# Kernel optimization log

Measured on AMD Instinct MI355X. Metric: run time of the kernel, lower is better.

The kernel has to match this reference:

```python
import jax, jax.numpy as jnp
import numpy as np

RES = 256      # cubic grid resolution
CH = 16        # feature channels
RR = 8         # reduced_res = ceil(log2(RES))
MASK = 128     # low-frequency mask size
N_PTS = 262144 # query points


def _bilinear(feat, gx, gy):
    """torch.F.grid_sample, bilinear, align_corners=True, zero padding.
    feat: (C,H,W); gx,gy: (N,) in [-1,1] (gx indexes W, gy indexes H).
    Returns (N,C)."""
    H, W = feat.shape[1], feat.shape[2]
    x = (gx + 1.0) * 0.5 * (W - 1)
    y = (gy + 1.0) * 0.5 * (H - 1)
    x0 = jnp.floor(x)
    y0 = jnp.floor(y)
    wx = x - x0
    wy = y - y0
    x0i = jnp.clip(x0.astype(jnp.int32), 0, W - 1)
    x1i = jnp.clip(x0i + 1, 0, W - 1)
    y0i = jnp.clip(y0.astype(jnp.int32), 0, H - 1)
    y1i = jnp.clip(y0i + 1, 0, H - 1)
    v00 = feat[:, y0i, x0i]
    v01 = feat[:, y0i, x1i]
    v10 = feat[:, y1i, x0i]
    v11 = feat[:, y1i, x1i]
    out = (v00 * (1 - wx) * (1 - wy) + v01 * wx * (1 - wy)
           + v10 * (1 - wx) * wy + v11 * wx * wy)  # (C,N)
    return out.T


def _plane(P, mask2d, gx, gy, icoord):
    """One phasor plane: mask -> ifft2 -> grid_sample -> Fourier integration.
    P: (CH*RR, RES, RES, 2); returns (N, CH)."""
    Pc = (P[..., 0] + 1j * P[..., 1]) * mask2d          # (C,H,W) complex
    Pc = jnp.fft.ifft2(Pc)                              # ifft over last 2 axes
    C = P.shape[0]
    # interleave (real, imag) per complex channel, like permute+reshape in torch
    feat = jnp.stack([Pc.real, Pc.imag], axis=1).reshape(2 * C, RES, RES)
    samp = _bilinear(feat, gx, gy).reshape(-1, 2 * CH, RR)  # (N, 2*CH, RR)
    Z = samp[:, :CH] + 1j * samp[:, CH:]                    # (N, CH, RR)
    s = (icoord + 1.0) * 0.5 * (2 ** RR - 1)                # scaled coord
    coef = 2.0 ** jnp.arange(RR) - 1.0                      # (RR,)
    basis = jnp.exp(2j * jnp.pi * s[:, None] * coef / (2 ** RR))  # (N, RR)
    return jnp.einsum('nr,ncr->nc', basis, Z).real


def _forward(Pu, Pv, Pw, inputs):
    mask2d = jnp.zeros((RES, RES), jnp.float32).at[:MASK, :MASK].set(1.0)
    out = (_plane(Pu, mask2d, inputs[:, 1], inputs[:, 2], inputs[:, 0])
           + _plane(Pv, mask2d, inputs[:, 0], inputs[:, 2], inputs[:, 1])
           + _plane(Pw, mask2d, inputs[:, 0], inputs[:, 1], inputs[:, 2]))
    return out  # (N, CH)


def setup_inputs() -> dict:
    key = jax.random.key(0)
    k1, k2, k3, k4 = jax.random.split(key, 4)
    Pu = 0.001 * jax.random.normal(k1, (CH * RR, RES, RES, 2), jnp.float32)
    Pv = 0.001 * jax.random.normal(k2, (CH * RR, RES, RES, 2), jnp.float32)
    Pw = 0.001 * jax.random.normal(k3, (CH * RR, RES, RES, 2), jnp.float32)
    inputs = jax.random.uniform(k4, (N_PTS, 3), jnp.float32, -1.0, 1.0)
    return {"Pu": Pu, "Pv": Pv, "Pw": Pw, "inputs": inputs}


def reference(Pu, Pv, Pw, inputs):
    return _forward(Pu, Pv, Pw, inputs)
```

## Files before the change

kernel.cpp:

```cpp
#include <hip/hip_runtime.h>
#include <hip/hip_bf16.h>
#include <cmath>


#define NPTS 262144

typedef float vf2 __attribute__((ext_vector_type(2)));

__device__ __forceinline__ int brev8(int x) { return (int)(__brev((unsigned)x) >> 24); }

__device__ __forceinline__ unsigned pack_bf16(float2 v) {
    unsigned short a = __builtin_bit_cast(unsigned short, __float2bfloat16(v.x));
    unsigned short b = __builtin_bit_cast(unsigned short, __float2bfloat16(v.y));
    return (unsigned)a | ((unsigned)b << 16);
}
__device__ __forceinline__ float2 unpack_bf16(unsigned u) {
    return make_float2(__uint_as_float(u << 16), __uint_as_float(u & 0xffff0000u));
}
__device__ __forceinline__ vf2 up2(unsigned u) {
    vf2 r; r.x = __uint_as_float(u << 16); r.y = __uint_as_float(u & 0xffff0000u);
    return r;
}

__device__ __forceinline__ void plane_coords(int p, float in0, float in1, float in2,
                                             float& gx, float& gy, float& sc) {
    gx = (p == 0) ? in1 : in0;
    gy = (p == 2) ? in1 : in2;
    sc = (p == 0) ? in0 : ((p == 1) ? in1 : in2);
}

__global__ __launch_bounds__(512) void pass1_kernel(const float* __restrict__ P0,
                                                    const float* __restrict__ P1,
                                                    const float* __restrict__ P2,
                                                    unsigned* __restrict__ X) {
    __shared__ float2 tw[128];
    __shared__ float2 tile[256 * 17];

    int t = threadIdx.x;
    if (t < 128) {
        float s, c;
        sincospif((float)t * (1.0f / 128.0f), &s, &c);
        tw[t] = make_float2(c, s);
    }
    int plane = blockIdx.y;
    const float* P = (plane == 0) ? P0 : ((plane == 1) ? P1 : P2);
    unsigned* Xp = X + (size_t)plane * 4194304;

    int b  = blockIdx.x;
    int ch = b >> 3;
    int x0 = (b & 7) << 4;
    const float* src = P + (size_t)ch * 131072 + x0 * 2;

    const float scale = 1.0f / 65536.0f;
#pragma unroll
    for (int k = 0; k < 2; k++) {
        int i = t + (k << 9);
        int y = i >> 3;
        int j = i & 7;
        float4 v = *(const float4*)(src + (size_t)y * 512 + (j << 2));
        float2 c0 = make_float2(v.x * scale, v.y * scale);
        float2 c1 = make_float2(v.z * scale, v.w * scale);
        int pos = brev8(y);
        tile[pos * 17 + 2 * j]           = c0;
        tile[(pos + 1) * 17 + 2 * j]     = c0;
        tile[pos * 17 + 2 * j + 1]       = c1;
        tile[(pos + 1) * 17 + 2 * j + 1] = c1;
    }
    __syncthreads();

    int w = t >> 6, l = t & 63;
    int col = (w << 1) + (l & 1);
    int bb  = l >> 1;
#pragma unroll
    for (int s = 2; s <= 8; s++) {
        int half = 1 << (s - 1);
#pragma unroll
        for (int k = 0; k < 4; k++) {
            int bf = bb + (k << 5);
            int j  = bf & (half - 1);
            int g  = bf >> (s - 1);
            int i0 = (g << s) + j;
            int i1 = i0 + half;
            float2 u = tile[i0 * 17 + col];
            float2 v = tile[i1 * 17 + col];
            float2 wq = tw[j << (8 - s)];
            float2 vt = make_float2(v.x * wq.x - v.y * wq.y, v.x * wq.y + v.y * wq.x);
            tile[i0 * 17 + col] = make_float2(u.x + vt.x, u.y + vt.y);
            tile[i1 * 17 + col] = make_float2(u.x - vt.x, u.y - vt.y);
        }
    }
    __syncthreads();

    unsigned* dst = Xp + (size_t)ch * 32768 + x0;
#pragma unroll
    for (int k = 0; k < 8; k++) {
        int i = t + (k << 9);
        int v = i >> 4;
        int c = i & 15;
        dst[(size_t)v * 128 + c] = pack_bf16(tile[v * 17 + c]);
    }
}

__global__ __launch_bounds__(1024) void pass2_kernel(const unsigned* __restrict__ X,
                                                     __hip_bfloat16* __restrict__ feat) {
    __shared__ float2 tw[128];
    __shared__ float2 rows[16 * 257];

    int t = threadIdx.x;
    if (t < 128) {
        float s, c;
        sincospif((float)t * (1.0f / 128.0f), &s, &c);
        tw[t] = make_float2(c, s);
    }
    int w = t >> 6;
    int l = t & 63;
    int v   = blockIdx.x & 255;
    int g   = blockIdx.x >> 8;
    int ch0 = g << 4;
    int ch  = ch0 + w;
    int plane = blockIdx.y;
    const unsigned* Xp = X + (size_t)plane * 4194304;
    __hip_bfloat16* fp = feat + (size_t)plane * 16777216;

    const uint2* src = (const uint2*)(Xp + ((size_t)ch * 256 + v) * 128);
    uint2 d = src[l];
    float2 c0 = unpack_bf16(d.x);
    float2 c1 = unpack_bf16(d.y);
    float2* row = rows + w * 257;
    int p0 = brev8(2 * l);
    int p1 = brev8(2 * l + 1);
    row[p0]     = c0;
    row[p0 + 1] = c0;
    row[p1]     = c1;
    row[p1 + 1] = c1;
    __syncthreads();
#pragma unroll
    for (int s = 2; s <= 8; s++) {
        int half = 1 << (s - 1);
#pragma unroll
        for (int k = 0; k < 2; k++) {
            int bf = l + (k << 6);
            int j  = bf & (half - 1);
            int gg = bf >> (s - 1);
            int i0 = (gg << s) + j;
            int i1 = i0 + half;
            float2 u  = row[i0];
            float2 vv = row[i1];
            float2 wq = tw[j << (8 - s)];
            float2 vt = make_float2(vv.x * wq.x - vv.y * wq.y,
                                    vv.x * wq.y + vv.y * wq.x);
            row[i0] = make_float2(u.x + vt.x, u.y + vt.y);
            row[i1] = make_float2(u.x - vt.x, u.y - vt.y);
        }
    }
    __syncthreads();
    __hip_bfloat16* dst = fp + (size_t)v * 65536 + (ch0 << 1);
#pragma unroll
    for (int k = 0; k < 8; k++) {
        int f = t + (k << 10);
        int x = f >> 5;
        int j = f & 31;
        float2 cpx = rows[(j >> 1) * 257 + x];
        float val = (j & 1) ? cpx.y : cpx.x;
        dst[x * 256 + j] = __float2bfloat16(val);
    }
}

__device__ __forceinline__ int tile_key(float gx, float gy) {
    float xf = (gx + 1.0f) * 127.5f;
    float yf = (gy + 1.0f) * 127.5f;
    int x0 = max(0, min((int)floorf(xf), 255));
    int y0 = max(0, min((int)floorf(yf), 255));
    return (y0 & 0xF0) | (x0 >> 4);
}

__global__ __launch_bounds__(1024) void hist_kernel(const float* __restrict__ pts,
                                                    unsigned* __restrict__ hist) {
    __shared__ unsigned hb[256];
    int t = threadIdx.x;
    int p = blockIdx.y;
    int n = (blockIdx.x << 10) + t;
    if (t < 256) hb[t] = 0;
    __syncthreads();
    float in0 = pts[3 * n + 0], in1 = pts[3 * n + 1], in2 = pts[3 * n + 2];
    float gx, gy, sc;
    plane_coords(p, in0, in1, in2, gx, gy, sc);
    atomicAdd(&hb[tile_key(gx, gy)], 1u);
    __syncthreads();
    if (t < 256 && hb[t]) atomicAdd(&hist[(p << 8) + t], hb[t]);
}

__global__ __launch_bounds__(256) void scan_kernel(const unsigned* __restrict__ hist,
                                                   unsigned* __restrict__ cursor) {
    __shared__ unsigned s[256];
    int t = threadIdx.x;
    for (int p = 0; p < 3; p++) {
        unsigned v = hist[(p << 8) + t];
        s[t] = v;
        __syncthreads();
#pragma unroll
        for (int d = 1; d < 256; d <<= 1) {
            unsigned add = (t >= d) ? s[t - d] : 0u;
            __syncthreads();
            s[t] += add;
            __syncthreads();
        }
        cursor[(p << 8) + t] = s[t] - v;
        __syncthreads();
    }
}

__global__ __launch_bounds__(1024) void scatter_kernel(const float* __restrict__ pts,
                                                       unsigned* __restrict__ cursor,
                                                       float4* __restrict__ psort) {
    __shared__ unsigned cnt[256];
    __shared__ unsigned base[256];
    int t = threadIdx.x;
    int p = blockIdx.y;
    int n = (blockIdx.x << 10) + t;
    if (t < 256) cnt[t] = 0;
    __syncthreads();
    float in0 = pts[3 * n + 0], in1 = pts[3 * n + 1], in2 = pts[3 * n + 2];
    float gx, gy, sc;
    plane_coords(p, in0, in1, in2, gx, gy, sc);
    int key = tile_key(gx, gy);
    unsigned rank = atomicAdd(&cnt[key], 1u);
    __syncthreads();
    if (t < 256 && cnt[t]) base[t] = atomicAdd(&cursor[(p << 8) + t], cnt[t]);
    __syncthreads();
    psort[p * NPTS + base[key] + rank] = make_float4(gx, gy, sc, __int_as_float(n));
}

__global__ __launch_bounds__(256) void gather_kernel(const ushort* __restrict__ feat,
                                                     const float4* __restrict__ psort,
                                                     float* __restrict__ partial) {
    int t = threadIdx.x;
    int w = t >> 6;
    int l = t & 63;
    int h = l >> 5;
    int q = l & 31;
    int p = blockIdx.y;
    const ushort* fb = feat + (size_t)p * 16777216;

    int b  = blockIdx.x;
    int lb = ((b & 7) << 12) | (b >> 3);
    int idx = (lb << 3) + (w << 1) + h;
    float4 pt = psort[p * NPTS + idx];
    float gx = pt.x, gy = pt.y, sc = pt.z;
    int n = __float_as_int(pt.w);

    float xf = (gx + 1.0f) * 127.5f;
    float yf = (gy + 1.0f) * 127.5f;
    float x0f = floorf(xf);
    float y0f = floorf(yf);
    float wx = xf - x0f;
    float wy = yf - y0f;
    int x0 = max(0, min((int)x0f, 255));
    int y0 = max(0, min((int)y0f, 255));
    int dx = (x0 < 255) ? 256 : 0;
    int dy = (y0 < 255) ? 65536 : 0;

    const ushort* bp = fb + (((y0 << 8) + x0) << 8) + (q << 3);
    uint4 d00 = *(const uint4*)bp;
    uint4 d01 = *(const uint4*)(bp + dx);
    uint4 d10 = *(const uint4*)(bp + dy);
    uint4 d11 = *(const uint4*)(bp + dx + dy);

    float coef = (float)((1 << (q & 7)) - 1);
    float a = (sc + 1.0f) * 0.99609375f * coef;
    float sn, cs;
    sincospif(a, &sn, &cs);
    float merged = (q < 16) ? cs : -sn;
    float wr0 = __shfl(merged, (l & 48) + 0);
    float wr1 = __shfl(merged, (l & 48) + 1);
    float wr2 = __shfl(merged, (l & 48) + 2);
    float wr3 = __shfl(merged, (l & 48) + 3);
    float wr4 = __shfl(merged, (l & 48) + 4);
    float wr5 = __shfl(merged, (l & 48) + 5);
    float wr6 = __shfl(merged, (l & 48) + 6);
    float wr7 = __shfl(merged, (l & 48) + 7);

    float w00 = (1.0f - wx) * (1.0f - wy);
    float w01 = wx * (1.0f - wy);
    float w10 = (1.0f - wx) * wy;
    float w11 = wx * wy;

    vf2 b0 = w00 * up2(d00.x) + w01 * up2(d01.x) + w10 * up2(d10.x) + w11 * up2(d11.x);
    vf2 b1 = w00 * up2(d00.y) + w01 * up2(d01.y) + w10 * up2(d10.y) + w11 * up2(d11.y);
    vf2 b2 = w00 * up2(d00.z) + w01 * up2(d01.z) + w10 * up2(d10.z) + w11 * up2(d11.z);
    vf2 b3 = w00 * up2(d00.w) + w01 * up2(d01.w) + w10 * up2(d10.w) + w11 * up2(d11.w);

    vf2 wa; wa.x = wr0; wa.y = wr1;
    vf2 wb; wb.x = wr2; wb.y = wr3;
    vf2 wc; wc.x = wr4; wc.y = wr5;
    vf2 wd; wd.x = wr6; wd.y = wr7;
    vf2 acc2 = b0 * wa + b1 * wb + b2 * wc + b3 * wd;
    float acc = acc2.x + acc2.y;

    acc += __shfl_xor(acc, 16);
    if (q < 16) {
        partial[(((size_t)p * NPTS + n) << 4) + q] = acc;
    }
}

__global__ __launch_bounds__(256) void combine_kernel(const float4* __restrict__ pa,
                                                      float4* __restrict__ out) {
    int i = (blockIdx.x << 8) + threadIdx.x;
    float4 a = pa[i];
    float4 b = pa[i + 1048576];
    float4 c = pa[i + 2097152];
    out[i] = make_float4(a.x + b.x + c.x, a.y + b.y + c.y,
                         a.z + b.z + c.z, a.w + b.w + c.w);
}

extern "C" void kernel_launch(void* const* d_in, const int* in_sizes, int n_in,
                              void* d_out, int out_size, void* d_ws, size_t ws_size,
                              hipStream_t stream) {
    const float* P0  = (const float*)d_in[0];
    const float* P1  = (const float*)d_in[1];
    const float* P2  = (const float*)d_in[2];
    const float* pts = (const float*)d_in[3];
    float* out = (float*)d_out;
    char* ws = (char*)d_ws;

    __hip_bfloat16* feat = (__hip_bfloat16*)ws;
    unsigned* X          = (unsigned*)(ws + 100663296u);
    float*    partial    = (float*)(ws + 150994944u);
    float4*   psort      = (float4*)(ws + 201326592u);
    unsigned* hist       = (unsigned*)(ws + 213909504u);
    unsigned* cursor     = (unsigned*)(ws + 213912576u);

    hipMemsetAsync(hist, 0, 3072, stream);

    dim3 g1(1024, 3);
    pass1_kernel<<<g1, 512, 0, stream>>>(P0, P1, P2, X);
    dim3 g2(2048, 3);
    pass2_kernel<<<g2, 1024, 0, stream>>>(X, feat);

    dim3 gs(256, 3);
    hist_kernel<<<gs, 1024, 0, stream>>>(pts, hist);
    scan_kernel<<<1, 256, 0, stream>>>(hist, cursor);
    scatter_kernel<<<gs, 1024, 0, stream>>>(pts, cursor, psort);

    dim3 gg(32768, 3);
    gather_kernel<<<gg, 256, 0, stream>>>((const ushort*)feat, psort, partial);
    combine_kernel<<<4096, 256, 0, stream>>>((const float4*)partial, (float4*)out);
}
```

Before: 398.3 us.

## Store features as scaled fp16, use dot2 in gather, atomically accumulate output

```diff
diff --git a/kernel.cpp b/kernel.cpp
--- a/kernel.cpp
+++ b/kernel.cpp
@@ -1,11 +1,12 @@
 #include <hip/hip_runtime.h>
 #include <hip/hip_bf16.h>
+#include <hip/hip_fp16.h>
 #include <cmath>
 
 
 #define NPTS 262144
 
-typedef float vf2 __attribute__((ext_vector_type(2)));
+typedef _Float16 f16x2 __attribute__((ext_vector_type(2)));
 
 __device__ __forceinline__ int brev8(int x) { return (int)(__brev((unsigned)x) >> 24); }
 
@@ -17,9 +18,16 @@
 __device__ __forceinline__ float2 unpack_bf16(unsigned u) {
     return make_float2(__uint_as_float(u << 16), __uint_as_float(u & 0xffff0000u));
 }
-__device__ __forceinline__ vf2 up2(unsigned u) {
-    vf2 r; r.x = __uint_as_float(u << 16); r.y = __uint_as_float(u & 0xffff0000u);
-    return r;
+
+__device__ __forceinline__ float dot2f(unsigned a, unsigned b, float c) {
+#if __has_builtin(__builtin_amdgcn_fdot2)
+    return __builtin_amdgcn_fdot2(__builtin_bit_cast(f16x2, a),
+                                  __builtin_bit_cast(f16x2, b), c, false);
+#else
+    float d;
+    asm("v_dot2_f32_f16 %0, %1, %2, %3" : "=v"(d) : "v"(a), "v"(b), "v"(c));
+    return d;
+#endif
 }
 
 __device__ __forceinline__ void plane_coords(int p, float in0, float in1, float in2,
@@ -102,7 +110,7 @@
 }
 
 __global__ __launch_bounds__(1024) void pass2_kernel(const unsigned* __restrict__ X,
-                                                     __hip_bfloat16* __restrict__ feat) {
+                                                     __half* __restrict__ feat) {
     __shared__ float2 tw[128];
     __shared__ float2 rows[16 * 257];
 
@@ -120,7 +128,7 @@
     int ch  = ch0 + w;
     int plane = blockIdx.y;
     const unsigned* Xp = X + (size_t)plane * 4194304;
-    __hip_bfloat16* fp = feat + (size_t)plane * 16777216;
+    __half* fp = feat + (size_t)plane * 16777216;
 
     const uint2* src = (const uint2*)(Xp + ((size_t)ch * 256 + v) * 128);
     uint2 d = src[l];
@@ -154,7 +162,7 @@
         }
     }
     __syncthreads();
-    __hip_bfloat16* dst = fp + (size_t)v * 65536 + (ch0 << 1);
+    __half* dst = fp + (size_t)v * 65536 + (ch0 << 1);
 #pragma unroll
     for (int k = 0; k < 8; k++) {
         int f = t + (k << 10);
@@ -162,7 +170,7 @@
         int j = f & 31;
         float2 cpx = rows[(j >> 1) * 257 + x];
         float val = (j & 1) ? cpx.y : cpx.x;
-        dst[x * 256 + j] = __float2bfloat16(val);
+        dst[x * 256 + j] = __float2half(val * 16384.0f);
     }
 }
 
@@ -223,31 +231,6 @@
     float in0 = pts[3 * n + 0], in1 = pts[3 * n + 1], in2 = pts[3 * n + 2];
     float gx, gy, sc;
     plane_coords(p, in0, in1, in2, gx, gy, sc);
-    int key = tile_key(gx, gy);
-    unsigned rank = atomicAdd(&cnt[key], 1u);
-    __syncthreads();
-    if (t < 256 && cnt[t]) base[t] = atomicAdd(&cursor[(p << 8) + t], cnt[t]);
-    __syncthreads();
-    psort[p * NPTS + base[key] + rank] = make_float4(gx, gy, sc, __int_as_float(n));
-}
-
-__global__ __launch_bounds__(256) void gather_kernel(const ushort* __restrict__ feat,
-                                                     const float4* __restrict__ psort,
-                                                     float* __restrict__ partial) {
-    int t = threadIdx.x;
-    int w = t >> 6;
-    int l = t & 63;
-    int h = l >> 5;
-    int q = l & 31;
-    int p = blockIdx.y;
-    const ushort* fb = feat + (size_t)p * 16777216;
-
-    int b  = blockIdx.x;
-    int lb = ((b & 7) << 12) | (b >> 3);
-    int idx = (lb << 3) + (w << 1) + h;
-    float4 pt = psort[p * NPTS + idx];
-    float gx = pt.x, gy = pt.y, sc = pt.z;
-    int n = __float_as_int(pt.w);
 
     float xf = (gx + 1.0f) * 127.5f;
     float yf = (gy + 1.0f) * 127.5f;
@@ -257,60 +240,91 @@
     float wy = yf - y0f;
     int x0 = max(0, min((int)x0f, 255));
     int y0 = max(0, min((int)y0f, 255));
-    int dx = (x0 < 255) ? 256 : 0;
-    int dy = (y0 < 255) ? 65536 : 0;
-
-    const ushort* bp = fb + (((y0 << 8) + x0) << 8) + (q << 3);
+    int key = (y0 & 0xF0) | (x0 >> 4);
+
+    unsigned rank = atomicAdd(&cnt[key], 1u);
+    __syncthreads();
+    if (t < 256 && cnt[t]) base[t] = atomicAdd(&cursor[(p << 8) + t], cnt[t]);
+    __syncthreads();
+
+    unsigned pk = ((unsigned)((y0 << 8) + x0) << 8)
+                | ((x0 < 255) ? (1u << 24) : 0u)
+                | ((y0 < 255) ? (1u << 25) : 0u);
+    float sprime = (sc + 1.0f) * 0.99609375f;
+    __half2 wh = __floats2half2_rn(wx, wy);
+    psort[p * NPTS + base[key] + rank] =
+        make_float4(__uint_as_float(pk), __builtin_bit_cast(float, wh),
+                    sprime, __int_as_float(n));
+}
+
+__global__ __launch_bounds__(256) void gather_kernel(const ushort* __restrict__ feat,
+                                                     const float4* __restrict__ psort,
+                                                     float* __restrict__ out) {
+    int t = threadIdx.x;
+    int w = t >> 6;
+    int l = t & 63;
+    int h = l >> 5;
+    int q = l & 31;
+    int p = blockIdx.y;
+    const ushort* fb = feat + (size_t)p * 16777216;
+
+    int b  = blockIdx.x;
+    int lb = ((b & 7) << 12) | (b >> 3);
+    int idx = (lb << 3) + (w << 1) + h;
+    float4 pt = psort[p * NPTS + idx];
+
+    unsigned pk = __float_as_uint(pt.x);
+    __half2 wh = __builtin_bit_cast(__half2, pt.y);
+    float wx = __low2float(wh);
+    float wy = __high2float(wh);
+    float s1 = pt.z;
+    int n = __float_as_int(pt.w);
+
+    unsigned bpoff = pk & 0xFFFFFFu;
+    int dx = (int)((pk >> 16) & 0x100u);
+    int dy = (int)((pk >> 9) & 0x10000u);
+
+    const ushort* bp = fb + bpoff + (q << 3);
     uint4 d00 = *(const uint4*)bp;
     uint4 d01 = *(const uint4*)(bp + dx);
     uint4 d10 = *(const uint4*)(bp + dy);
     uint4 d11 = *(const uint4*)(bp + dx + dy);
 
     float coef = (float)((1 << (q & 7)) - 1);
-    float a = (sc + 1.0f) * 0.99609375f * coef;
+    float a = s1 * coef;
     float sn, cs;
     sincospif(a, &sn, &cs);
     float merged = (q < 16) ? cs : -sn;
-    float wr0 = __shfl(merged, (l & 48) + 0);
-    float wr1 = __shfl(merged, (l & 48) + 1);
-    float wr2 = __shfl(merged, (l & 48) + 2);
-    float wr3 = __shfl(merged, (l & 48) + 3);
-    float wr4 = __shfl(merged, (l & 48) + 4);
-    float wr5 = __shfl(merged, (l & 48) + 5);
-    float wr6 = __shfl(merged, (l & 48) + 6);
-    float wr7 = __shfl(merged, (l & 48) + 7);
-
-    float w00 = (1.0f - wx) * (1.0f - wy);
-    float w01 = wx * (1.0f - wy);
-    float w10 = (1.0f - wx) * wy;
-    float w11 = wx * wy;
-
-    vf2 b0 = w00 * up2(d00.x) + w01 * up2(d01.x) + w10 * up2(d10.x) + w11 * up2(d11.x);
-    vf2 b1 = w00 * up2(d00.y) + w01 * up2(d01.y) + w10 * up2(d10.y) + w11 * up2(d11.y);
-    vf2 b2 = w00 * up2(d00.z) + w01 * up2(d01.z) + w10 * up2(d10.z) + w11 * up2(d11.z);
-    vf2 b3 = w00 * up2(d00.w) + w01 * up2(d01.w) + w10 * up2(d10.w) + w11 * up2(d11.w);
-
-    vf2 wa; wa.x = wr0; wa.y = wr1;
-    vf2 wb; wb.x = wr2; wb.y = wr3;
-    vf2 wc; wc.x = wr4; wc.y = wr5;
-    vf2 wd; wd.x = wr6; wd.y = wr7;
-    vf2 acc2 = b0 * wa + b1 * wb + b2 * wc + b3 * wd;
-    float acc = acc2.x + acc2.y;
-
-    acc += __shfl_xor(acc, 16);
+    float partner = __int_as_float(
+        __builtin_amdgcn_ds_swizzle(__float_as_int(merged), 0x041F));
+    float lo = (l & 1) ? partner : merged;
+    float hi = (l & 1) ? merged : partner;
+    __half2 wp = __floats2half2_rn(lo, hi);
+    unsigned wpi = __builtin_bit_cast(unsigned, wp);
+    unsigned w0 = (unsigned)__builtin_amdgcn_ds_swizzle((int)wpi, 0x0010);
+    unsigned w1 = (unsigned)__builtin_amdgcn_ds_swizzle((int)wpi, 0x0050);
+    unsigned w2 = (unsigned)__builtin_amdgcn_ds_swizzle((int)wpi, 0x0090);
+    unsigned w3 = (unsigned)__builtin_amdgcn_ds_swizzle((int)wpi, 0x00D0);
+
+    float s00 = dot2f(d00.w, w3, dot2f(d00.z, w2, dot2f(d00.y, w1, dot2f(d00.x, w0, 0.0f))));
+    float s01 = dot2f(d01.w, w3, dot2f(d01.z, w2, dot2f(d01.y, w1, dot2f(d01.x, w0, 0.0f))));
+    float s10 = dot2f(d10.w, w3, dot2f(d10.z, w2, dot2f(d10.y, w1, dot2f(d10.x, w0, 0.0f))));
+    float s11 = dot2f(d11.w, w3, dot2f(d11.z, w2, dot2f(d11.y, w1, dot2f(d11.x, w0, 0.0f))));
+
+    const float INV = 6.103515625e-05f;
+    float wys = wy * INV;
+    float wyc = INV - wys;
+    float wxc = 1.0f - wx;
+    float acc = s00 * (wxc * wyc);
+    acc = fmaf(s01, wx * wyc, acc);
+    acc = fmaf(s10, wxc * wys, acc);
+    acc = fmaf(s11, wx * wys, acc);
+
+    acc += __int_as_float(
+        __builtin_amdgcn_ds_swizzle(__float_as_int(acc), 0x401F));
     if (q < 16) {
-        partial[(((size_t)p * NPTS + n) << 4) + q] = acc;
-    }
-}
-
-__global__ __launch_bounds__(256) void combine_kernel(const float4* __restrict__ pa,
-                                                      float4* __restrict__ out) {
-    int i = (blockIdx.x << 8) + threadIdx.x;
-    float4 a = pa[i];
-    float4 b = pa[i + 1048576];
-    float4 c = pa[i + 2097152];
-    out[i] = make_float4(a.x + b.x + c.x, a.y + b.y + c.y,
-                         a.z + b.z + c.z, a.w + b.w + c.w);
+        atomicAdd(&out[((size_t)n << 4) + q], acc);
+    }
 }
 
 extern "C" void kernel_launch(void* const* d_in, const int* in_sizes, int n_in,
@@ -323,14 +337,14 @@
     float* out = (float*)d_out;
     char* ws = (char*)d_ws;
 
-    __hip_bfloat16* feat = (__hip_bfloat16*)ws;
-    unsigned* X          = (unsigned*)(ws + 100663296u);
-    float*    partial    = (float*)(ws + 150994944u);
-    float4*   psort      = (float4*)(ws + 201326592u);
-    unsigned* hist       = (unsigned*)(ws + 213909504u);
-    unsigned* cursor     = (unsigned*)(ws + 213912576u);
+    __half*   feat   = (__half*)ws;
+    unsigned* X      = (unsigned*)(ws + 100663296u);
+    float4*   psort  = (float4*)(ws + 201326592u);
+    unsigned* hist   = (unsigned*)(ws + 213909504u);
+    unsigned* cursor = (unsigned*)(ws + 213912576u);
 
     hipMemsetAsync(hist, 0, 3072, stream);
+    hipMemsetAsync(out, 0, (size_t)NPTS * 64, stream);
 
     dim3 g1(1024, 3);
     pass1_kernel<<<g1, 512, 0, stream>>>(P0, P1, P2, X);
@@ -343,6 +357,5 @@
     scatter_kernel<<<gs, 1024, 0, stream>>>(pts, cursor, psort);
 
     dim3 gg(32768, 3);
-    gather_kernel<<<gg, 256, 0, stream>>>((const ushort*)feat, psort, partial);
-    combine_kernel<<<4096, 256, 0, stream>>>((const float4*)partial, (float4*)out);
-}
+    gather_kernel<<<gg, 256, 0, stream>>>((const ushort*)feat, psort, out);
+}
```

After: 389.6 us. 1.02x faster.
